# Optimization experiments

Hardware: AMD Instinct MI355X
Metric: run time of the kernel (lower is better)

## Reference

```python
import jax, jax.numpy as jnp
import numpy as np

B, L, K, D = 1024, 50, 20, 64
N_ITEMS, N_USERS = 100000, 10000
ALPHA = 0.2


def setup_inputs() -> dict:
    key = jax.random.key(0)
    k1, k2, k3, k4, k5, k6 = jax.random.split(key, 6)
    item_table = jax.random.normal(k1, (N_ITEMS, D), jnp.float32) * 0.02
    user_table = jax.random.normal(k2, (N_USERS, D), jnp.float32) * 0.02
    # kaiming_uniform_ on a (B,K,D) tensor: bound = sqrt(6 / fan_in), fan_in = K*D
    bound = float(np.sqrt(6.0 / (K * D)))
    memory_init = jax.random.uniform(k3, (B, K, D), jnp.float32, -bound, bound)
    user_id = jax.random.randint(k4, (B,), 0, N_USERS)
    seq = jax.random.randint(k5, (B, L), 0, N_ITEMS)
    seq_length = jax.random.randint(k6, (B,), 0, L + 1)
    return {
        "item_table": item_table,
        "user_table": user_table,
        "memory_init": memory_init,
        "user_id": user_id,
        "seq": seq,
        "seq_length": seq_length,
    }


def reference(item_table, user_table, memory_init, user_id, seq, seq_length):
    item_emb = item_table[seq]                      # (B, L, D)

    def step(mem, e):                                # mem: (B,K,D), e: (B,D)
        # read: attention over memory slots
        z = jax.nn.softmax(jnp.einsum('bkd,bd->bk', mem, e), axis=1)
        # write: rank-1 erase/add update
        erase = jax.nn.sigmoid(e)[:, None, :]        # (B,1,D)
        add = jnp.tanh(e)[:, None, :]                # (B,1,D)
        zc = z[:, :, None]                           # (B,K,1)
        new_mem = mem * (1.0 - zc * erase) + zc * add
        return new_mem, new_mem

    _, mems = jax.lax.scan(step, memory_init, jnp.swapaxes(item_emb, 0, 1))
    stacked = jnp.concatenate([memory_init[None], mems], axis=0)  # (L+1, B, K, D)
    # gather memory state at each user's sequence length
    mem_emb = stacked[seq_length, jnp.arange(B)]     # (B, K, D)

    last = item_table[seq[:, -1]]                    # (B, D)
    z = jax.nn.softmax(jnp.einsum('bd,bkd->bk', last, mem_emb), axis=-1)
    p = jnp.einsum('bk,bkd->bd', z, mem_emb)         # (B, D)
    pu = user_table[user_id] + ALPHA * p             # (B, D)
    scores = pu @ item_table.T                       # (B, N_ITEMS)
    return scores
```

## Files before the change

kernel.cpp:

```cpp
#include <hip/hip_runtime.h>
#include <hip/hip_bf16.h>

#define B_ 1024
#define L_ 50
#define K_ 20
#define D_ 64
#define N_ITEMS 100000
#define ALPHA 0.2f

typedef __bf16 bf16x8 __attribute__((ext_vector_type(8)));
typedef float f32x4 __attribute__((ext_vector_type(4)));

__device__ __forceinline__ unsigned short f2b(float f) {
    union { float f; unsigned int u; } x; x.f = f;
    unsigned int r = (x.u + 0x7FFFu + ((x.u >> 16) & 1u)) >> 16;
    return (unsigned short)r;
}

__global__ void convert_kernel(const float* __restrict__ in,
                               unsigned short* __restrict__ out, int n4) {
    int i = blockIdx.x * blockDim.x + threadIdx.x;
    if (i < n4) {
        float4 v = ((const float4*)in)[i];
        ushort4 o;
        o.x = f2b(v.x); o.y = f2b(v.y); o.z = f2b(v.z); o.w = f2b(v.w);
        ((ushort4*)out)[i] = o;
    }
}

__global__ __launch_bounds__(64) void recur_kernel(
    const float* __restrict__ item_table, const float* __restrict__ user_table,
    const float* __restrict__ memory_init, const int* __restrict__ user_id,
    const int* __restrict__ seq, const int* __restrict__ seq_len,
    unsigned short* __restrict__ pu_out) {
    const int b = blockIdx.x;
    const int lane = threadIdx.x;
    const int T = seq_len[b];
    float mem[K_];
#pragma unroll
    for (int k = 0; k < K_; ++k)
        mem[k] = memory_init[(b * K_ + k) * D_ + lane];

    const int* sq = seq + b * L_;
    float e_next = item_table[(size_t)sq[0] * D_ + lane];

    for (int t = 0; t < T; ++t) {
        float e = e_next;
        int tn = (t + 1 < L_) ? (t + 1) : t;
        e_next = item_table[(size_t)sq[tn] * D_ + lane];

        float w[K_];
#pragma unroll
        for (int k = 0; k < K_; ++k) w[k] = mem[k] * e;
#pragma unroll
        for (int off = 32; off > 0; off >>= 1) {
#pragma unroll
            for (int k = 0; k < K_; ++k) w[k] += __shfl_xor(w[k], off, 64);
        }
        float mx = w[0];
#pragma unroll
        for (int k = 1; k < K_; ++k) mx = fmaxf(mx, w[k]);
        float s = 0.0f;
#pragma unroll
        for (int k = 0; k < K_; ++k) { w[k] = __expf(w[k] - mx); s += w[k]; }
        float inv = 1.0f / s;
        float er = 1.0f / (1.0f + __expf(-e));
        float t2 = __expf(2.0f * e);
        float ad = (t2 - 1.0f) / (t2 + 1.0f);
#pragma unroll
        for (int k = 0; k < K_; ++k) {
            float z = w[k] * inv;
            mem[k] = mem[k] * (1.0f - z * er) + z * ad;
        }
    }

    float last = item_table[(size_t)sq[L_ - 1] * D_ + lane];
    float w[K_];
#pragma unroll
    for (int k = 0; k < K_; ++k) w[k] = mem[k] * last;
#pragma unroll
    for (int off = 32; off > 0; off >>= 1) {
#pragma unroll
        for (int k = 0; k < K_; ++k) w[k] += __shfl_xor(w[k], off, 64);
    }
    float mx = w[0];
#pragma unroll
    for (int k = 1; k < K_; ++k) mx = fmaxf(mx, w[k]);
    float s = 0.0f;
#pragma unroll
    for (int k = 0; k < K_; ++k) { w[k] = __expf(w[k] - mx); s += w[k]; }
    float inv = 1.0f / s;
    float p = 0.0f;
#pragma unroll
    for (int k = 0; k < K_; ++k) p += (w[k] * inv) * mem[k];

    float pu = user_table[(size_t)user_id[b] * D_ + lane] + ALPHA * p;
    pu_out[b * D_ + lane] = f2b(pu);
}

__global__ __launch_bounds__(256) void gemm_kernel(
    const unsigned short* __restrict__ itemb,
    const unsigned short* __restrict__ pub,
    float* __restrict__ out) {
    const int lane = threadIdx.x & 63;
    const int wv = threadIdx.x >> 6;
    const int r = lane & 15;
    const int q = lane >> 4;
    const int m0 = blockIdx.x * 256 + wv * 64;
    const int n0 = blockIdx.y * 64;

    bf16x8 a[4][2], bb[4][2];
#pragma unroll
    for (int sm = 0; sm < 4; ++sm) {
        const unsigned short* p = pub + (m0 + sm * 16 + r) * 64 + q * 8;
        a[sm][0] = *(const bf16x8*)(p);
        a[sm][1] = *(const bf16x8*)(p + 32);
    }
    bf16x8 zf;
#pragma unroll
    for (int i = 0; i < 8; ++i) zf[i] = (__bf16)0.0f;
#pragma unroll
    for (int sn = 0; sn < 4; ++sn) {
        int n = n0 + sn * 16 + r;
        if (n < N_ITEMS) {
            const unsigned short* p = itemb + (size_t)n * 64 + q * 8;
            bb[sn][0] = *(const bf16x8*)(p);
            bb[sn][1] = *(const bf16x8*)(p + 32);
        } else {
            bb[sn][0] = zf;
            bb[sn][1] = zf;
        }
    }

    f32x4 acc[4][4];
#pragma unroll
    for (int sm = 0; sm < 4; ++sm)
#pragma unroll
        for (int sn = 0; sn < 4; ++sn) {
            f32x4 c = {0.0f, 0.0f, 0.0f, 0.0f};
            c = __builtin_amdgcn_mfma_f32_16x16x32_bf16(a[sm][0], bb[sn][0], c, 0, 0, 0);
            c = __builtin_amdgcn_mfma_f32_16x16x32_bf16(a[sm][1], bb[sn][1], c, 0, 0, 0);
            acc[sm][sn] = c;
        }

#pragma unroll
    for (int sm = 0; sm < 4; ++sm)
#pragma unroll
        for (int sn = 0; sn < 4; ++sn) {
            int n = n0 + sn * 16 + r;
            if (n < N_ITEMS) {
                int mbase = m0 + sm * 16 + q * 4;
#pragma unroll
                for (int rr = 0; rr < 4; ++rr)
                    out[(size_t)(mbase + rr) * N_ITEMS + n] = acc[sm][sn][rr];
            }
        }
}

extern "C" void kernel_launch(void* const* d_in, const int* in_sizes, int n_in,
                              void* d_out, int out_size, void* d_ws, size_t ws_size,
                              hipStream_t stream) {
    const float* item_table  = (const float*)d_in[0];
    const float* user_table  = (const float*)d_in[1];
    const float* memory_init = (const float*)d_in[2];
    const int*   user_id     = (const int*)d_in[3];
    const int*   seq         = (const int*)d_in[4];
    const int*   seq_len     = (const int*)d_in[5];
    float* out = (float*)d_out;

    unsigned short* item_bf16 = (unsigned short*)d_ws;
    unsigned short* pu_bf16   = item_bf16 + (size_t)N_ITEMS * D_;

    int n4 = N_ITEMS * D_ / 4;
    convert_kernel<<<dim3((n4 + 255) / 256), dim3(256), 0, stream>>>(
        item_table, item_bf16, n4);
    recur_kernel<<<dim3(B_), dim3(64), 0, stream>>>(
        item_table, user_table, memory_init, user_id, seq, seq_len, pu_bf16);
    gemm_kernel<<<dim3(4, (N_ITEMS + 63) / 64), dim3(256), 0, stream>>>(
        item_bf16, pu_bf16, out);
}
```

Before: 561.5 us.

## Fuse bf16 conversion into recurrence launch, DPP reductions, swap GEMM operands for vector stores

The item-table conversion now runs as extra blocks inside the recurrence kernel, so the two overlap and one launch disappears. The wave reductions in the recurrence use DPP row operations plus readlane instead of shuffle butterflies. The GEMM swaps its MFMA operand roles so each lane holds four contiguous output columns, which allows 16-byte nontemporal stores in place of scalar strided stores. The output write is the dominant cost, so the store change is the main lever; the DPP reduction has to be exactly right to stay correct.

```diff
diff --git a/kernel.cpp b/kernel.cpp
--- a/kernel.cpp
+++ b/kernel.cpp
@@ -1,15 +1,17 @@
 #include <hip/hip_runtime.h>
-#include <hip/hip_bf16.h>
 
 #define B_ 1024
 #define L_ 50
 #define K_ 20
 #define D_ 64
 #define N_ITEMS 100000
+#define N4 (N_ITEMS * D_ / 4)
+#define CONV_BLOCKS 6250
 #define ALPHA 0.2f
 
 typedef __bf16 bf16x8 __attribute__((ext_vector_type(8)));
 typedef float f32x4 __attribute__((ext_vector_type(4)));
+typedef unsigned short u16x4 __attribute__((ext_vector_type(4)));
 
 __device__ __forceinline__ unsigned short f2b(float f) {
     union { float f; unsigned int u; } x; x.f = f;
@@ -17,22 +19,39 @@
     return (unsigned short)r;
 }
 
-__global__ void convert_kernel(const float* __restrict__ in,
-                               unsigned short* __restrict__ out, int n4) {
-    int i = blockIdx.x * blockDim.x + threadIdx.x;
-    if (i < n4) {
-        float4 v = ((const float4*)in)[i];
-        ushort4 o;
-        o.x = f2b(v.x); o.y = f2b(v.y); o.z = f2b(v.z); o.w = f2b(v.w);
-        ((ushort4*)out)[i] = o;
-    }
+#define DPP_ADD(x, ctrl, rmask, bctrl)                                        \
+    x += __int_as_float(__builtin_amdgcn_update_dpp(                          \
+        0, __float_as_int(x), ctrl, rmask, 0xF, bctrl))
+
+__device__ __forceinline__ float wave_sum_u(float x) {
+    DPP_ADD(x, 0x111, 0xF, true);
+    DPP_ADD(x, 0x112, 0xF, true);
+    DPP_ADD(x, 0x114, 0xF, true);
+    DPP_ADD(x, 0x118, 0xF, true);
+    DPP_ADD(x, 0x142, 0xA, false);
+    DPP_ADD(x, 0x143, 0xC, false);
+    return __int_as_float(__builtin_amdgcn_readlane(__float_as_int(x), 63));
 }
 
-__global__ __launch_bounds__(64) void recur_kernel(
+__global__ __launch_bounds__(64) void fused_front_kernel(
     const float* __restrict__ item_table, const float* __restrict__ user_table,
     const float* __restrict__ memory_init, const int* __restrict__ user_id,
     const int* __restrict__ seq, const int* __restrict__ seq_len,
-    unsigned short* __restrict__ pu_out) {
+    unsigned short* __restrict__ item_bf16, unsigned short* __restrict__ pu_out) {
+
+    if (blockIdx.x >= B_) {
+        int i = (int)(blockIdx.x - B_) * 64 + (int)threadIdx.x;
+        const int stride = CONV_BLOCKS * 64;
+#pragma unroll 4
+        for (; i < N4; i += stride) {
+            f32x4 v = __builtin_nontemporal_load((const f32x4*)item_table + i);
+            u16x4 o;
+            o.x = f2b(v.x); o.y = f2b(v.y); o.z = f2b(v.z); o.w = f2b(v.w);
+            ((u16x4*)item_bf16)[i] = o;
+        }
+        return;
+    }
+
     const int b = blockIdx.x;
     const int lane = threadIdx.x;
     const int T = seq_len[b];
@@ -51,12 +70,7 @@
 
         float w[K_];
 #pragma unroll
-        for (int k = 0; k < K_; ++k) w[k] = mem[k] * e;
-#pragma unroll
-        for (int off = 32; off > 0; off >>= 1) {
-#pragma unroll
-            for (int k = 0; k < K_; ++k) w[k] += __shfl_xor(w[k], off, 64);
-        }
+        for (int k = 0; k < K_; ++k) w[k] = wave_sum_u(mem[k] * e);
         float mx = w[0];
 #pragma unroll
         for (int k = 1; k < K_; ++k) mx = fmaxf(mx, w[k]);
@@ -77,12 +91,7 @@
     float last = item_table[(size_t)sq[L_ - 1] * D_ + lane];
     float w[K_];
 #pragma unroll
-    for (int k = 0; k < K_; ++k) w[k] = mem[k] * last;
-#pragma unroll
-    for (int off = 32; off > 0; off >>= 1) {
-#pragma unroll
-        for (int k = 0; k < K_; ++k) w[k] += __shfl_xor(w[k], off, 64);
-    }
+    for (int k = 0; k < K_; ++k) w[k] = wave_sum_u(mem[k] * last);
     float mx = w[0];
 #pragma unroll
     for (int k = 1; k < K_; ++k) mx = fmaxf(mx, w[k]);
@@ -109,52 +118,47 @@
     const int m0 = blockIdx.x * 256 + wv * 64;
     const int n0 = blockIdx.y * 64;
 
-    bf16x8 a[4][2], bb[4][2];
-#pragma unroll
-    for (int sm = 0; sm < 4; ++sm) {
-        const unsigned short* p = pub + (m0 + sm * 16 + r) * 64 + q * 8;
-        a[sm][0] = *(const bf16x8*)(p);
-        a[sm][1] = *(const bf16x8*)(p + 32);
-    }
     bf16x8 zf;
 #pragma unroll
     for (int i = 0; i < 8; ++i) zf[i] = (__bf16)0.0f;
+
+    bf16x8 ai[4][2];
 #pragma unroll
     for (int sn = 0; sn < 4; ++sn) {
         int n = n0 + sn * 16 + r;
         if (n < N_ITEMS) {
             const unsigned short* p = itemb + (size_t)n * 64 + q * 8;
-            bb[sn][0] = *(const bf16x8*)(p);
-            bb[sn][1] = *(const bf16x8*)(p + 32);
+            ai[sn][0] = *(const bf16x8*)(p);
+            ai[sn][1] = *(const bf16x8*)(p + 32);
         } else {
-            bb[sn][0] = zf;
-            bb[sn][1] = zf;
+            ai[sn][0] = zf;
+            ai[sn][1] = zf;
         }
     }
-
-    f32x4 acc[4][4];
+    bf16x8 bp[4][2];
 #pragma unroll
-    for (int sm = 0; sm < 4; ++sm)
-#pragma unroll
-        for (int sn = 0; sn < 4; ++sn) {
-            f32x4 c = {0.0f, 0.0f, 0.0f, 0.0f};
-            c = __builtin_amdgcn_mfma_f32_16x16x32_bf16(a[sm][0], bb[sn][0], c, 0, 0, 0);
-            c = __builtin_amdgcn_mfma_f32_16x16x32_bf16(a[sm][1], bb[sn][1], c, 0, 0, 0);
-            acc[sm][sn] = c;
-        }
+    for (int sm = 0; sm < 4; ++sm) {
+        const unsigned short* p = pub + (m0 + sm * 16 + r) * 64 + q * 8;
+        bp[sm][0] = *(const bf16x8*)(p);
+        bp[sm][1] = *(const bf16x8*)(p + 32);
+    }
 
 #pragma unroll
-    for (int sm = 0; sm < 4; ++sm)
+    for (int sn = 0; sn < 4; ++sn) {
+        int nb = n0 + sn * 16 + q * 4;
+        bool ok = (n0 + sn * 16) < N_ITEMS;
 #pragma unroll
-        for (int sn = 0; sn < 4; ++sn) {
-            int n = n0 + sn * 16 + r;
-            if (n < N_ITEMS) {
-                int mbase = m0 + sm * 16 + q * 4;
-#pragma unroll
-                for (int rr = 0; rr < 4; ++rr)
-                    out[(size_t)(mbase + rr) * N_ITEMS + n] = acc[sm][sn][rr];
+        for (int sm = 0; sm < 4; ++sm) {
+            f32x4 c = {0.0f, 0.0f, 0.0f, 0.0f};
+            c = __builtin_amdgcn_mfma_f32_16x16x32_bf16(ai[sn][0], bp[sm][0], c, 0, 0, 0);
+            c = __builtin_amdgcn_mfma_f32_16x16x32_bf16(ai[sn][1], bp[sm][1], c, 0, 0, 0);
+            if (ok) {
+                int m = m0 + sm * 16 + r;
+                __builtin_nontemporal_store(
+                    c, (f32x4*)(out + (size_t)m * N_ITEMS + nb));
             }
         }
+    }
 }
 
 extern "C" void kernel_launch(void* const* d_in, const int* in_sizes, int n_in,
@@ -171,11 +175,9 @@
     unsigned short* item_bf16 = (unsigned short*)d_ws;
     unsigned short* pu_bf16   = item_bf16 + (size_t)N_ITEMS * D_;
 
-    int n4 = N_ITEMS * D_ / 4;
-    convert_kernel<<<dim3((n4 + 255) / 256), dim3(256), 0, stream>>>(
-        item_table, item_bf16, n4);
-    recur_kernel<<<dim3(B_), dim3(64), 0, stream>>>(
-        item_table, user_table, memory_init, user_id, seq, seq_len, pu_bf16);
+    fused_front_kernel<<<dim3(B_ + CONV_BLOCKS), dim3(64), 0, stream>>>(
+        item_table, user_table, memory_init, user_id, seq, seq_len,
+        item_bf16, pu_bf16);
     gemm_kernel<<<dim3(4, (N_ITEMS + 63) / 64), dim3(256), 0, stream>>>(
         item_bf16, pu_bf16, out);
 }
```

Measured after the change: 574.5 us. 1.02x slower.
